# Optimization experiments

Hardware: AMD Instinct MI355X
Metric: run time of the kernel (lower is better)

Reference implementation:

```python
import jax, jax.numpy as jnp
import numpy as np

MAX_STEP = 20

def setup_inputs() -> dict:
    key = jax.random.key(0)
    k1, k2 = jax.random.split(key)
    B, L, E, H = 32, 2048, 256, 256
    word_rep = jax.random.normal(k1, (B, L, E), dtype=jnp.float32)
    # nn.Parameter(torch.randn(...).uniform_(-0.1, 0.1)) -> uniform in [-0.1, 0.1]
    cnn = jax.random.uniform(k2, (MAX_STEP, E, H), dtype=jnp.float32, minval=-0.1, maxval=0.1)
    return {"word_rep": word_rep, "cnn": cnn}

def reference(word_rep, cnn):
    # word_rep: [B, L, E]; cnn: [MAX_STEP, E, H]
    L = word_rep.shape[1]
    # Gather the cyclically-indexed per-position weight: [L, E, H]
    W = cnn[jnp.arange(L) % MAX_STEP]
    # Fused batched matmul over all positions at once: [B, L, H]
    hidden_vecs = jnp.einsum('ble,leh->blh', word_rep, W)
    return (hidden_vecs, hidden_vecs[:, -1])
```

## Files before the change

kernel.cpp:

```cpp
#include <hip/hip_runtime.h>
#include <hip/hip_bf16.h>

#define B_ 32
#define L_ 2048
#define E_ 256
#define H_ 256
#define MAXSTEP 20
#define NL 4
#define NCHUNK 26

typedef __attribute__((ext_vector_type(4))) float f32x4;
typedef __attribute__((ext_vector_type(8))) short bf16x8;
using bf16 = __hip_bfloat16;

__device__ inline short cvt1(float x) {
    bf16 b = __float2bfloat16(x);
    return *reinterpret_cast<short*>(&b);
}

__global__ void transpose_w_kernel(const float* __restrict__ cnn, short* __restrict__ wt) {
    __shared__ short tile[32][33];
    const int s  = blockIdx.z;
    const int e0 = blockIdx.y * 32;
    const int h0 = blockIdx.x * 32;
    const int tx = threadIdx.x;
    const int ty = threadIdx.y;
    const float* src = cnn + ((size_t)s * E_ + e0) * H_ + h0;
#pragma unroll
    for (int i = ty; i < 32; i += 8)
        tile[i][tx] = cvt1(src[(size_t)i * H_ + tx]);
    __syncthreads();
    short* dst = wt + ((size_t)s * H_ + h0) * E_ + e0;
#pragma unroll
    for (int i = ty; i < 32; i += 8)
        dst[(size_t)i * E_ + tx] = tile[tx][i];
}

__global__ __launch_bounds__(256, 2) void vaw_sames_kernel(
        const float* __restrict__ A, const short* __restrict__ Wt,
        float* __restrict__ out) {
    __shared__ __align__(16) float aLds[2][B_ * E_];

    const int s     = blockIdx.x / NCHUNK;
    const int chunk = blockIdx.x % NCHUNK;
    const int cnt   = (s < 8) ? 103 : 102;
    const int wv    = threadIdx.x >> 6;
    const int lane  = threadIdx.x & 63;
    const int r     = lane & 15;
    const int g     = lane >> 4;
    const int nbase = wv * 64;
    const int key   = r & 7;

    const short* wtb = Wt + ((size_t)s * H_ + nbase + r) * E_ + g * 8;
    bf16x8 breg[8][4];
#pragma unroll
    for (int kk = 0; kk < 8; ++kk)
#pragma unroll
        for (int nf = 0; nf < 4; ++nf)
            breg[kk][nf] = *(const bf16x8*)(wtb + (size_t)nf * 16 * E_ + kk * 32);

    auto lof = [&](int it) {
        int idx = chunk * NL + it;
        if (idx > cnt - 1) idx = cnt - 1;
        return s + 20 * idx;
    };

    auto stage = [&](int it) {
        const int l = lof(it);
        float* dst = aLds[it & 1];
#pragma unroll
        for (int t = 0; t < 8; ++t) {
            const int b  = t * 4 + wv;
            const int cg = lane ^ (b & 7);
            const float* gp = A + ((size_t)b * L_ + l) * E_ + cg * 4;
            __builtin_amdgcn_global_load_lds(
                (const __attribute__((address_space(1))) void*)gp,
                (__attribute__((address_space(3))) void*)&dst[b * 256],
                16, 0, 0);
        }
    };

    stage(0);

#pragma unroll
    for (int it = 0; it < NL; ++it) {
        const int l   = lof(it);
        const int cur = it & 1;

        if (it < NL - 1) stage(it + 1);
        if (it == 0)           asm volatile("s_waitcnt vmcnt(8)"  ::: "memory");
        else if (it < NL - 1)  asm volatile("s_waitcnt vmcnt(40)" ::: "memory");
        else                   asm volatile("s_waitcnt vmcnt(32)" ::: "memory");
        __builtin_amdgcn_s_barrier();
        __builtin_amdgcn_sched_barrier(0);

        f32x4 acc[2][4] = {};
#pragma unroll
        for (int kk = 0; kk < 8; ++kk) {
            const int c0 = kk * 8 + g * 2;
            f32x4 a0lo = *(const f32x4*)&aLds[cur][r * 256 + ((c0 ^ key) << 2)];
            f32x4 a0hi = *(const f32x4*)&aLds[cur][r * 256 + (((c0 + 1) ^ key) << 2)];
            f32x4 a1lo = *(const f32x4*)&aLds[cur][(r + 16) * 256 + ((c0 ^ key) << 2)];
            f32x4 a1hi = *(const f32x4*)&aLds[cur][(r + 16) * 256 + (((c0 + 1) ^ key) << 2)];
            bf16x8 a0, a1;
#pragma unroll
            for (int j = 0; j < 4; ++j) {
                a0[j]     = cvt1(a0lo[j]);
                a0[j + 4] = cvt1(a0hi[j]);
                a1[j]     = cvt1(a1lo[j]);
                a1[j + 4] = cvt1(a1hi[j]);
            }
#pragma unroll
            for (int nf = 0; nf < 4; ++nf) {
                acc[0][nf] = __builtin_amdgcn_mfma_f32_16x16x32_bf16(a0, breg[kk][nf], acc[0][nf], 0, 0, 0);
                acc[1][nf] = __builtin_amdgcn_mfma_f32_16x16x32_bf16(a1, breg[kk][nf], acc[1][nf], 0, 0, 0);
            }
        }

        const int row0 = g * 4;
#pragma unroll
        for (int mf = 0; mf < 2; ++mf) {
#pragma unroll
            for (int nf = 0; nf < 4; ++nf) {
                const int h = nbase + nf * 16 + r;
#pragma unroll
                for (int i = 0; i < 4; ++i) {
                    const int bb = mf * 16 + row0 + i;
                    out[((size_t)bb * L_ + l) * H_ + h] = acc[mf][nf][i];
                }
            }
        }
        if (l == L_ - 1) {
            float* out2 = out + (size_t)B_ * L_ * H_;
#pragma unroll
            for (int mf = 0; mf < 2; ++mf)
#pragma unroll
                for (int nf = 0; nf < 4; ++nf) {
                    const int h = nbase + nf * 16 + r;
#pragma unroll
                    for (int i = 0; i < 4; ++i) {
                        const int bb = mf * 16 + row0 + i;
                        out2[(size_t)bb * H_ + h] = acc[mf][nf][i];
                    }
                }
        }

        __builtin_amdgcn_s_barrier();
    }
}

__global__ __launch_bounds__(256) void vaw_fallback_kernel(
        const float* __restrict__ A, const float* __restrict__ W, float* __restrict__ out) {
    __shared__ __align__(16) float aLds[2][B_ * E_];
    const int l0   = blockIdx.x * NL;
    const int wv   = threadIdx.x >> 6;
    const int lane = threadIdx.x & 63;
    const int r    = lane & 15;
    const int g    = lane >> 4;
    const int nbase = wv * 64;
    const int key   = r & 7;

    auto stage = [&](int it) {
        float* dst = aLds[it & 1];
        const int l = l0 + it;
#pragma unroll
        for (int t = 0; t < 8; ++t) {
            const int b  = t * 4 + wv;
            const int cg = lane ^ (b & 7);
            const float* gp = A + ((size_t)b * L_ + l) * E_ + cg * 4;
            __builtin_amdgcn_global_load_lds(
                (const __attribute__((address_space(1))) void*)gp,
                (__attribute__((address_space(3))) void*)&dst[b * 256],
                16, 0, 0);
        }
    };

    stage(0);
#pragma unroll 1
    for (int it = 0; it < NL; ++it) {
        const int l   = l0 + it;
        const int sidx = l % MAXSTEP;
        const int cur = it & 1;
        if (it < NL - 1) {
            stage(it + 1);
            asm volatile("s_waitcnt vmcnt(8)" ::: "memory");
        } else {
            asm volatile("s_waitcnt vmcnt(0)" ::: "memory");
        }
        __builtin_amdgcn_s_barrier();
        __builtin_amdgcn_sched_barrier(0);

        f32x4 acc[2][4] = {};
        const float* Wf = W + (size_t)sidx * E_ * H_;
#pragma unroll 2
        for (int kk = 0; kk < 8; ++kk) {
            const int k0 = kk * 32;
            const int c0 = kk * 8 + g * 2;
            f32x4 a0lo = *(const f32x4*)&aLds[cur][r * 256 + ((c0 ^ key) << 2)];
            f32x4 a0hi = *(const f32x4*)&aLds[cur][r * 256 + (((c0 + 1) ^ key) << 2)];
            f32x4 a1lo = *(const f32x4*)&aLds[cur][(r + 16) * 256 + ((c0 ^ key) << 2)];
            f32x4 a1hi = *(const f32x4*)&aLds[cur][(r + 16) * 256 + (((c0 + 1) ^ key) << 2)];
            bf16x8 a0, a1;
#pragma unroll
            for (int j = 0; j < 4; ++j) {
                a0[j]     = cvt1(a0lo[j]);
                a0[j + 4] = cvt1(a0hi[j]);
                a1[j]     = cvt1(a1lo[j]);
                a1[j + 4] = cvt1(a1hi[j]);
            }
            bf16x8 b0, b1, b2, b3;
#pragma unroll
            for (int j = 0; j < 8; ++j) {
                const size_t krow = (size_t)(k0 + g * 8 + j) * H_;
                b0[j] = cvt1(Wf[krow + nbase +  0 + r]);
                b1[j] = cvt1(Wf[krow + nbase + 16 + r]);
                b2[j] = cvt1(Wf[krow + nbase + 32 + r]);
                b3[j] = cvt1(Wf[krow + nbase + 48 + r]);
            }
            acc[0][0] = __builtin_amdgcn_mfma_f32_16x16x32_bf16(a0, b0, acc[0][0], 0, 0, 0);
            acc[0][1] = __builtin_amdgcn_mfma_f32_16x16x32_bf16(a0, b1, acc[0][1], 0, 0, 0);
            acc[0][2] = __builtin_amdgcn_mfma_f32_16x16x32_bf16(a0, b2, acc[0][2], 0, 0, 0);
            acc[0][3] = __builtin_amdgcn_mfma_f32_16x16x32_bf16(a0, b3, acc[0][3], 0, 0, 0);
            acc[1][0] = __builtin_amdgcn_mfma_f32_16x16x32_bf16(a1, b0, acc[1][0], 0, 0, 0);
            acc[1][1] = __builtin_amdgcn_mfma_f32_16x16x32_bf16(a1, b1, acc[1][1], 0, 0, 0);
            acc[1][2] = __builtin_amdgcn_mfma_f32_16x16x32_bf16(a1, b2, acc[1][2], 0, 0, 0);
            acc[1][3] = __builtin_amdgcn_mfma_f32_16x16x32_bf16(a1, b3, acc[1][3], 0, 0, 0);
        }

        const int row0 = g * 4;
#pragma unroll
        for (int mf = 0; mf < 2; ++mf)
#pragma unroll
            for (int nf = 0; nf < 4; ++nf) {
                const int h = nbase + nf * 16 + r;
#pragma unroll
                for (int i = 0; i < 4; ++i) {
                    const int bb = mf * 16 + row0 + i;
                    out[((size_t)bb * L_ + l) * H_ + h] = acc[mf][nf][i];
                }
            }
        if (l == L_ - 1) {
            float* out2 = out + (size_t)B_ * L_ * H_;
#pragma unroll
            for (int mf = 0; mf < 2; ++mf)
#pragma unroll
                for (int nf = 0; nf < 4; ++nf) {
                    const int h = nbase + nf * 16 + r;
#pragma unroll
                    for (int i = 0; i < 4; ++i) {
                        const int bb = mf * 16 + row0 + i;
                        out2[(size_t)bb * H_ + h] = acc[mf][nf][i];
                    }
                }
        }
        __builtin_amdgcn_s_barrier();
    }
}

extern "C" void kernel_launch(void* const* d_in, const int* in_sizes, int n_in,
                              void* d_out, int out_size, void* d_ws, size_t ws_size,
                              hipStream_t stream) {
    const float* word_rep = (const float*)d_in[0];
    const float* cnn      = (const float*)d_in[1];
    float* out = (float*)d_out;

    const size_t wt_bytes = (size_t)MAXSTEP * E_ * H_ * sizeof(short);
    if (ws_size >= wt_bytes) {
        short* wt = (short*)d_ws;
        transpose_w_kernel<<<dim3(8, 8, 20), dim3(32, 8), 0, stream>>>(cnn, wt);
        vaw_sames_kernel<<<dim3(MAXSTEP * NCHUNK), dim3(256), 0, stream>>>(word_rep, wt, out);
    } else {
        vaw_fallback_kernel<<<dim3(L_ / NL), dim3(256), 0, stream>>>(word_rep, cnn, out);
    }
}
```

Baseline: 45.03 us.

## Split A staging into K-halves with triple-buffered LDS pipeline

Each position's activation tile is now staged in two halves along E (128 columns each) and rotated through three LDS buffers, with loads issued two stages ahead. Accumulators persist across the two halves, and results are stored only after the second half. LDS use per block drops from 64KB to 48KB, and load latency gets more overlap with MFMA work. The cost is twice as many barrier and wait steps per position, plus hand-tuned vmcnt values that must match exactly.

```diff
diff --git a/kernel.cpp b/kernel.cpp
--- a/kernel.cpp
+++ b/kernel.cpp
@@ -39,7 +39,7 @@
 __global__ __launch_bounds__(256, 2) void vaw_sames_kernel(
         const float* __restrict__ A, const short* __restrict__ Wt,
         float* __restrict__ out) {
-    __shared__ __align__(16) float aLds[2][B_ * E_];
+    __shared__ __align__(16) float aLds[3][B_ * 128];
 
     const int s     = blockIdx.x / NCHUNK;
     const int chunk = blockIdx.x % NCHUNK;
@@ -59,49 +59,67 @@
         for (int nf = 0; nf < 4; ++nf)
             breg[kk][nf] = *(const bf16x8*)(wtb + (size_t)nf * 16 * E_ + kk * 32);
 
-    auto lof = [&](int it) {
-        int idx = chunk * NL + it;
+    auto lof = [&](int il) {
+        int idx = chunk * NL + il;
         if (idx > cnt - 1) idx = cnt - 1;
         return s + 20 * idx;
     };
 
-    auto stage = [&](int it) {
-        const int l = lof(it);
-        float* dst = aLds[it & 1];
-#pragma unroll
-        for (int t = 0; t < 8; ++t) {
-            const int b  = t * 4 + wv;
-            const int cg = lane ^ (b & 7);
-            const float* gp = A + ((size_t)b * L_ + l) * E_ + cg * 4;
+    auto stage = [&](int t) {
+        const int l  = lof(t >> 1);
+        const int hk = t & 1;
+        float* dst = aLds[t % 3];
+        const int local = lane & 31;
+        const int half  = lane >> 5;
+#pragma unroll
+        for (int j = 0; j < 4; ++j) {
+            const int r0  = j * 8 + wv * 2;
+            const int row = r0 + half;
+            const int cg  = local ^ (row & 7);
+            const float* gp = A + ((size_t)row * L_ + l) * E_ + hk * 128 + cg * 4;
             __builtin_amdgcn_global_load_lds(
                 (const __attribute__((address_space(1))) void*)gp,
-                (__attribute__((address_space(3))) void*)&dst[b * 256],
+                (__attribute__((address_space(3))) void*)&dst[r0 * 128],
                 16, 0, 0);
         }
     };
 
     stage(0);
-
-#pragma unroll
-    for (int it = 0; it < NL; ++it) {
-        const int l   = lof(it);
-        const int cur = it & 1;
-
-        if (it < NL - 1) stage(it + 1);
-        if (it == 0)           asm volatile("s_waitcnt vmcnt(8)"  ::: "memory");
-        else if (it < NL - 1)  asm volatile("s_waitcnt vmcnt(40)" ::: "memory");
-        else                   asm volatile("s_waitcnt vmcnt(32)" ::: "memory");
+    stage(1);
+
+    f32x4 acc[2][4];
+
+#pragma unroll
+    for (int t = 0; t < 2 * NL; ++t) {
+        const int cur = t % 3;
+        const int hk  = t & 1;
+        const int l   = lof(t >> 1);
+
+        if (t < 2 * NL - 2) stage(t + 2);
+
+        if (t < 2)                asm volatile("s_waitcnt vmcnt(8)"  ::: "memory");
+        else if (t < 2 * NL - 2)  asm volatile("s_waitcnt vmcnt(40)" ::: "memory");
+        else if (t == 2 * NL - 2) asm volatile("s_waitcnt vmcnt(36)" ::: "memory");
+        else                      asm volatile("s_waitcnt vmcnt(32)" ::: "memory");
         __builtin_amdgcn_s_barrier();
         __builtin_amdgcn_sched_barrier(0);
 
-        f32x4 acc[2][4] = {};
-#pragma unroll
-        for (int kk = 0; kk < 8; ++kk) {
-            const int c0 = kk * 8 + g * 2;
-            f32x4 a0lo = *(const f32x4*)&aLds[cur][r * 256 + ((c0 ^ key) << 2)];
-            f32x4 a0hi = *(const f32x4*)&aLds[cur][r * 256 + (((c0 + 1) ^ key) << 2)];
-            f32x4 a1lo = *(const f32x4*)&aLds[cur][(r + 16) * 256 + ((c0 ^ key) << 2)];
-            f32x4 a1hi = *(const f32x4*)&aLds[cur][(r + 16) * 256 + (((c0 + 1) ^ key) << 2)];
+        if (hk == 0) {
+#pragma unroll
+            for (int mf = 0; mf < 2; ++mf)
+#pragma unroll
+                for (int nf = 0; nf < 4; ++nf)
+                    acc[mf][nf] = f32x4{0.f, 0.f, 0.f, 0.f};
+        }
+
+#pragma unroll
+        for (int kkh = 0; kkh < 4; ++kkh) {
+            const int kk = hk * 4 + kkh;
+            const int c0 = kkh * 8 + g * 2;
+            f32x4 a0lo = *(const f32x4*)&aLds[cur][r * 128 + ((c0 ^ key) << 2)];
+            f32x4 a0hi = *(const f32x4*)&aLds[cur][r * 128 + (((c0 + 1) ^ key) << 2)];
+            f32x4 a1lo = *(const f32x4*)&aLds[cur][(r + 16) * 128 + ((c0 ^ key) << 2)];
+            f32x4 a1hi = *(const f32x4*)&aLds[cur][(r + 16) * 128 + (((c0 + 1) ^ key) << 2)];
             bf16x8 a0, a1;
 #pragma unroll
             for (int j = 0; j < 4; ++j) {
@@ -117,32 +135,34 @@
             }
         }
 
-        const int row0 = g * 4;
-#pragma unroll
-        for (int mf = 0; mf < 2; ++mf) {
-#pragma unroll
-            for (int nf = 0; nf < 4; ++nf) {
-                const int h = nbase + nf * 16 + r;
-#pragma unroll
-                for (int i = 0; i < 4; ++i) {
-                    const int bb = mf * 16 + row0 + i;
-                    out[((size_t)bb * L_ + l) * H_ + h] = acc[mf][nf][i];
-                }
-            }
-        }
-        if (l == L_ - 1) {
-            float* out2 = out + (size_t)B_ * L_ * H_;
-#pragma unroll
-            for (int mf = 0; mf < 2; ++mf)
+        if (hk == 1) {
+            const int row0 = g * 4;
+#pragma unroll
+            for (int mf = 0; mf < 2; ++mf) {
 #pragma unroll
                 for (int nf = 0; nf < 4; ++nf) {
                     const int h = nbase + nf * 16 + r;
 #pragma unroll
                     for (int i = 0; i < 4; ++i) {
                         const int bb = mf * 16 + row0 + i;
-                        out2[(size_t)bb * H_ + h] = acc[mf][nf][i];
+                        out[((size_t)bb * L_ + l) * H_ + h] = acc[mf][nf][i];
                     }
                 }
+            }
+            if (l == L_ - 1) {
+                float* out2 = out + (size_t)B_ * L_ * H_;
+#pragma unroll
+                for (int mf = 0; mf < 2; ++mf)
+#pragma unroll
+                    for (int nf = 0; nf < 4; ++nf) {
+                        const int h = nbase + nf * 16 + r;
+#pragma unroll
+                        for (int i = 0; i < 4; ++i) {
+                            const int bb = mf * 16 + row0 + i;
+                            out2[(size_t)bb * H_ + h] = acc[mf][nf][i];
+                        }
+                    }
+            }
         }
 
         __builtin_amdgcn_s_barrier();
```

Measured after the change: 48.75 us. 1.08x slower.

## Split GEMM into single-wave blocks with triple-buffered K-slice pipeline

Applied to the files above, without the earlier changes.

Replaces the 4-wave block with independent 64-thread blocks, each computing a 64-column slice of H, and streams A in 64-wide K slices through a three-deep LDS ring without block barriers. This is meant to raise occupancy, shrink LDS use and remove barrier stalls. Each wave now loads the full A rows itself, so global A reads are quadrupled. The last-position output is moved to a separate small copy kernel.

```diff
diff --git a/kernel.cpp b/kernel.cpp
--- a/kernel.cpp
+++ b/kernel.cpp
@@ -6,8 +6,8 @@
 #define E_ 256
 #define H_ 256
 #define MAXSTEP 20
-#define NL 4
-#define NCHUNK 26
+#define NLW 4
+#define NCH 26
 
 typedef __attribute__((ext_vector_type(4))) float f32x4;
 typedef __attribute__((ext_vector_type(8))) short bf16x8;
@@ -36,19 +36,28 @@
         dst[(size_t)i * E_ + tx] = tile[tx][i];
 }
 
-__global__ __launch_bounds__(256, 2) void vaw_sames_kernel(
+__global__ void copy_last_kernel(const float* __restrict__ out, float* __restrict__ out2) {
+    const int h = threadIdx.x;
+#pragma unroll
+    for (int b = 0; b < B_; ++b)
+        out2[(size_t)b * H_ + h] = out[((size_t)b * L_ + (L_ - 1)) * H_ + h];
+}
+
+__global__ __launch_bounds__(64, 2) void vaw_wave_kernel(
         const float* __restrict__ A, const short* __restrict__ Wt,
         float* __restrict__ out) {
-    __shared__ __align__(16) float aLds[2][B_ * E_];
-
-    const int s     = blockIdx.x / NCHUNK;
-    const int chunk = blockIdx.x % NCHUNK;
+    __shared__ __align__(16) float aLds[3][B_ * 64];
+
+    const int bid   = blockIdx.x;
+    const int cg    = bid & 3;
+    const int sc    = bid >> 2;
+    const int s     = sc / NCH;
+    const int chunk = sc % NCH;
     const int cnt   = (s < 8) ? 103 : 102;
-    const int wv    = threadIdx.x >> 6;
-    const int lane  = threadIdx.x & 63;
+    const int lane  = threadIdx.x;
     const int r     = lane & 15;
     const int g     = lane >> 4;
-    const int nbase = wv * 64;
+    const int nbase = cg * 64;
     const int key   = r & 7;
 
     const short* wtb = Wt + ((size_t)s * H_ + nbase + r) * E_ + g * 8;
@@ -59,100 +68,117 @@
         for (int nf = 0; nf < 4; ++nf)
             breg[kk][nf] = *(const bf16x8*)(wtb + (size_t)nf * 16 * E_ + kk * 32);
 
-    auto lof = [&](int it) {
-        int idx = chunk * NL + it;
+    auto lof = [&](int il) {
+        int idx = chunk * NLW + il;
         if (idx > cnt - 1) idx = cnt - 1;
         return s + 20 * idx;
     };
 
-    auto stage = [&](int it) {
-        const int l = lof(it);
-        float* dst = aLds[it & 1];
-#pragma unroll
-        for (int t = 0; t < 8; ++t) {
-            const int b  = t * 4 + wv;
-            const int cg = lane ^ (b & 7);
-            const float* gp = A + ((size_t)b * L_ + l) * E_ + cg * 4;
+    auto stage = [&](int td) {
+        const int l  = lof(td >> 2);
+        const int kq = td & 3;
+        float* dst = aLds[td % 3];
+        const int row = (lane >> 4);
+        const int cL  = lane & 15;
+#pragma unroll
+        for (int j = 0; j < 8; ++j) {
+            const int rr = j * 4 + row;
+            const int cG = cL ^ (rr & 7);
+            const float* gp = A + ((size_t)rr * L_ + l) * E_ + kq * 64 + cG * 4;
             __builtin_amdgcn_global_load_lds(
                 (const __attribute__((address_space(1))) void*)gp,
-                (__attribute__((address_space(3))) void*)&dst[b * 256],
+                (__attribute__((address_space(3))) void*)&dst[j * 4 * 64],
                 16, 0, 0);
         }
     };
 
     stage(0);
-
-#pragma unroll
-    for (int it = 0; it < NL; ++it) {
-        const int l   = lof(it);
-        const int cur = it & 1;
-
-        if (it < NL - 1) stage(it + 1);
-        if (it == 0)           asm volatile("s_waitcnt vmcnt(8)"  ::: "memory");
-        else if (it < NL - 1)  asm volatile("s_waitcnt vmcnt(40)" ::: "memory");
-        else                   asm volatile("s_waitcnt vmcnt(32)" ::: "memory");
-        __builtin_amdgcn_s_barrier();
-        __builtin_amdgcn_sched_barrier(0);
-
-        f32x4 acc[2][4] = {};
-#pragma unroll
-        for (int kk = 0; kk < 8; ++kk) {
-            const int c0 = kk * 8 + g * 2;
-            f32x4 a0lo = *(const f32x4*)&aLds[cur][r * 256 + ((c0 ^ key) << 2)];
-            f32x4 a0hi = *(const f32x4*)&aLds[cur][r * 256 + (((c0 + 1) ^ key) << 2)];
-            f32x4 a1lo = *(const f32x4*)&aLds[cur][(r + 16) * 256 + ((c0 ^ key) << 2)];
-            f32x4 a1hi = *(const f32x4*)&aLds[cur][(r + 16) * 256 + (((c0 + 1) ^ key) << 2)];
-            bf16x8 a0, a1;
-#pragma unroll
-            for (int j = 0; j < 4; ++j) {
-                a0[j]     = cvt1(a0lo[j]);
-                a0[j + 4] = cvt1(a0hi[j]);
-                a1[j]     = cvt1(a1lo[j]);
-                a1[j + 4] = cvt1(a1hi[j]);
-            }
-#pragma unroll
-            for (int nf = 0; nf < 4; ++nf) {
-                acc[0][nf] = __builtin_amdgcn_mfma_f32_16x16x32_bf16(a0, breg[kk][nf], acc[0][nf], 0, 0, 0);
-                acc[1][nf] = __builtin_amdgcn_mfma_f32_16x16x32_bf16(a1, breg[kk][nf], acc[1][nf], 0, 0, 0);
-            }
-        }
-
-        const int row0 = g * 4;
-#pragma unroll
-        for (int mf = 0; mf < 2; ++mf) {
-#pragma unroll
-            for (int nf = 0; nf < 4; ++nf) {
-                const int h = nbase + nf * 16 + r;
-#pragma unroll
-                for (int i = 0; i < 4; ++i) {
-                    const int bb = mf * 16 + row0 + i;
-                    out[((size_t)bb * L_ + l) * H_ + h] = acc[mf][nf][i];
-                }
-            }
-        }
-        if (l == L_ - 1) {
-            float* out2 = out + (size_t)B_ * L_ * H_;
-#pragma unroll
-            for (int mf = 0; mf < 2; ++mf)
+    stage(1);
+
+    f32x4 acc[2][4];
+
+#pragma unroll 1
+    for (int il = 0; il < NLW; ++il) {
+        const int l     = lof(il);
+        const bool first = (il == 0);
+        const bool last  = (il == NLW - 1);
+
+#pragma unroll
+        for (int q = 0; q < 4; ++q) {
+            const int t   = il * 4 + q;
+            const int buf = t % 3;
+
+            if (!last || q < 2) stage(t + 2);
+
+            if (q == 0) {
+                if (first) asm volatile("s_waitcnt vmcnt(16)" ::: "memory");
+                else       asm volatile("s_waitcnt vmcnt(48)" ::: "memory");
+            } else if (q == 1) {
+                if (first) asm volatile("s_waitcnt vmcnt(16)" ::: "memory");
+                else       asm volatile("s_waitcnt vmcnt(48)" ::: "memory");
+            } else if (q == 2) {
+                if (last)  asm volatile("s_waitcnt vmcnt(8)"  ::: "memory");
+                else       asm volatile("s_waitcnt vmcnt(16)" ::: "memory");
+            } else {
+                if (last)  asm volatile("s_waitcnt vmcnt(0)"  ::: "memory");
+                else       asm volatile("s_waitcnt vmcnt(16)" ::: "memory");
+            }
+            __builtin_amdgcn_sched_barrier(0);
+
+            if (q == 0) {
+#pragma unroll
+                for (int mf = 0; mf < 2; ++mf)
+#pragma unroll
+                    for (int nf = 0; nf < 4; ++nf)
+                        acc[mf][nf] = f32x4{0.f, 0.f, 0.f, 0.f};
+            }
+
+#pragma unroll
+            for (int kkh = 0; kkh < 2; ++kkh) {
+                const int kk = q * 2 + kkh;
+                const int c0 = kkh * 8 + g * 2;
+                f32x4 a0lo = *(const f32x4*)&aLds[buf][r * 64 + ((c0 ^ key) << 2)];
+                f32x4 a0hi = *(const f32x4*)&aLds[buf][r * 64 + (((c0 + 1) ^ key) << 2)];
+                f32x4 a1lo = *(const f32x4*)&aLds[buf][(r + 16) * 64 + ((c0 ^ key) << 2)];
+                f32x4 a1hi = *(const f32x4*)&aLds[buf][(r + 16) * 64 + (((c0 + 1) ^ key) << 2)];
+                bf16x8 a0, a1;
+#pragma unroll
+                for (int j = 0; j < 4; ++j) {
+                    a0[j]     = cvt1(a0lo[j]);
+                    a0[j + 4] = cvt1(a0hi[j]);
+                    a1[j]     = cvt1(a1lo[j]);
+                    a1[j + 4] = cvt1(a1hi[j]);
+                }
 #pragma unroll
                 for (int nf = 0; nf < 4; ++nf) {
-                    const int h = nbase + nf * 16 + r;
-#pragma unroll
-                    for (int i = 0; i < 4; ++i) {
-                        const int bb = mf * 16 + row0 + i;
-                        out2[(size_t)bb * H_ + h] = acc[mf][nf][i];
+                    acc[0][nf] = __builtin_amdgcn_mfma_f32_16x16x32_bf16(a0, breg[kk][nf], acc[0][nf], 0, 0, 0);
+                    acc[1][nf] = __builtin_amdgcn_mfma_f32_16x16x32_bf16(a1, breg[kk][nf], acc[1][nf], 0, 0, 0);
+                }
+            }
+
+            if (q == 3) {
+                const int row0 = g * 4;
+#pragma unroll
+                for (int mf = 0; mf < 2; ++mf) {
+#pragma unroll
+                    for (int nf = 0; nf < 4; ++nf) {
+                        const int h = nbase + nf * 16 + r;
+#pragma unroll
+                        for (int i = 0; i < 4; ++i) {
+                            const int bb = mf * 16 + row0 + i;
+                            out[((size_t)bb * L_ + l) * H_ + h] = acc[mf][nf][i];
+                        }
                     }
                 }
-        }
-
-        __builtin_amdgcn_s_barrier();
+            }
+        }
     }
 }
 
 __global__ __launch_bounds__(256) void vaw_fallback_kernel(
         const float* __restrict__ A, const float* __restrict__ W, float* __restrict__ out) {
     __shared__ __align__(16) float aLds[2][B_ * E_];
-    const int l0   = blockIdx.x * NL;
+    const int l0   = blockIdx.x * 4;
     const int wv   = threadIdx.x >> 6;
     const int lane = threadIdx.x & 63;
     const int r    = lane & 15;
@@ -166,8 +192,8 @@
 #pragma unroll
         for (int t = 0; t < 8; ++t) {
             const int b  = t * 4 + wv;
-            const int cg = lane ^ (b & 7);
-            const float* gp = A + ((size_t)b * L_ + l) * E_ + cg * 4;
+            const int cgx = lane ^ (b & 7);
+            const float* gp = A + ((size_t)b * L_ + l) * E_ + cgx * 4;
             __builtin_amdgcn_global_load_lds(
                 (const __attribute__((address_space(1))) void*)gp,
                 (__attribute__((address_space(3))) void*)&dst[b * 256],
@@ -177,11 +203,11 @@
 
     stage(0);
 #pragma unroll 1
-    for (int it = 0; it < NL; ++it) {
+    for (int it = 0; it < 4; ++it) {
         const int l   = l0 + it;
         const int sidx = l % MAXSTEP;
         const int cur = it & 1;
-        if (it < NL - 1) {
+        if (it < 3) {
             stage(it + 1);
             asm volatile("s_waitcnt vmcnt(8)" ::: "memory");
         } else {
@@ -268,8 +294,9 @@
     if (ws_size >= wt_bytes) {
         short* wt = (short*)d_ws;
         transpose_w_kernel<<<dim3(8, 8, 20), dim3(32, 8), 0, stream>>>(cnn, wt);
-        vaw_sames_kernel<<<dim3(MAXSTEP * NCHUNK), dim3(256), 0, stream>>>(word_rep, wt, out);
+        vaw_wave_kernel<<<dim3(MAXSTEP * NCH * 4), dim3(64), 0, stream>>>(word_rep, wt, out);
+        copy_last_kernel<<<dim3(1), dim3(256), 0, stream>>>(out, out + (size_t)B_ * L_ * H_);
     } else {
-        vaw_fallback_kernel<<<dim3(L_ / NL), dim3(256), 0, stream>>>(word_rep, cnn, out);
+        vaw_fallback_kernel<<<dim3(L_ / 4), dim3(256), 0, stream>>>(word_rep, cnn, out);
     }
 }
```

Measured after the change: 64.63 us. +43.5%, slower.

## Split columns across eight waves per block to cut weight registers per wave

Applied to the files above, without the earlier changes.

The main kernel now runs 512 threads (8 waves) per block, with each wave owning 32 output columns instead of 64. This halves the per-wave weight register footprint and accumulators so more waves can be resident. The activation tile is loaded with 4 rows per wave, two stages are prefetched before the weight registers are filled, and the wait counts are retuned to match. The trade-off is that each wave converts the same A fragments for half as many MFMAs, so LDS reads and fp32-to-bf16 conversion per FLOP double.

```diff
diff --git a/kernel.cpp b/kernel.cpp
--- a/kernel.cpp
+++ b/kernel.cpp
@@ -7,7 +7,8 @@
 #define H_ 256
 #define MAXSTEP 20
 #define NL 4
-#define NCHUNK 26
+#define NCH 26
+#define NGRP (MAXSTEP * NCH)
 
 typedef __attribute__((ext_vector_type(4))) float f32x4;
 typedef __attribute__((ext_vector_type(8))) short bf16x8;
@@ -36,31 +37,24 @@
         dst[(size_t)i * E_ + tx] = tile[tx][i];
 }
 
-__global__ __launch_bounds__(256, 2) void vaw_sames_kernel(
+__global__ __launch_bounds__(512, 4) void vaw_occ_kernel(
         const float* __restrict__ A, const short* __restrict__ Wt,
         float* __restrict__ out) {
     __shared__ __align__(16) float aLds[2][B_ * E_];
 
-    const int s     = blockIdx.x / NCHUNK;
-    const int chunk = blockIdx.x % NCHUNK;
+    const int g_    = blockIdx.x;
+    const int s     = g_ / NCH;
+    const int chunk = g_ % NCH;
     const int cnt   = (s < 8) ? 103 : 102;
     const int wv    = threadIdx.x >> 6;
     const int lane  = threadIdx.x & 63;
     const int r     = lane & 15;
     const int g     = lane >> 4;
-    const int nbase = wv * 64;
+    const int nbase = wv * 32;
     const int key   = r & 7;
 
-    const short* wtb = Wt + ((size_t)s * H_ + nbase + r) * E_ + g * 8;
-    bf16x8 breg[8][4];
-#pragma unroll
-    for (int kk = 0; kk < 8; ++kk)
-#pragma unroll
-        for (int nf = 0; nf < 4; ++nf)
-            breg[kk][nf] = *(const bf16x8*)(wtb + (size_t)nf * 16 * E_ + kk * 32);
-
-    auto lof = [&](int it) {
-        int idx = chunk * NL + it;
+    auto lof = [&](int il) {
+        int idx = chunk * NL + il;
         if (idx > cnt - 1) idx = cnt - 1;
         return s + 20 * idx;
     };
@@ -69,32 +63,47 @@
         const int l = lof(it);
         float* dst = aLds[it & 1];
 #pragma unroll
-        for (int t = 0; t < 8; ++t) {
-            const int b  = t * 4 + wv;
-            const int cg = lane ^ (b & 7);
-            const float* gp = A + ((size_t)b * L_ + l) * E_ + cg * 4;
+        for (int j = 0; j < 4; ++j) {
+            const int row = wv + j * 8;
+            const int cg  = lane ^ (row & 7);
+            const float* gp = A + ((size_t)row * L_ + l) * E_ + cg * 4;
             __builtin_amdgcn_global_load_lds(
                 (const __attribute__((address_space(1))) void*)gp,
-                (__attribute__((address_space(3))) void*)&dst[b * 256],
+                (__attribute__((address_space(3))) void*)&dst[row * 256],
                 16, 0, 0);
         }
     };
 
     stage(0);
-
-#pragma unroll
+    stage(1);
+
+    const short* wtb = Wt + ((size_t)s * H_ + nbase + r) * E_ + g * 8;
+    bf16x8 breg[8][2];
+#pragma unroll
+    for (int kk = 0; kk < 8; ++kk)
+#pragma unroll
+        for (int nf = 0; nf < 2; ++nf)
+            breg[kk][nf] = *(const bf16x8*)(wtb + (size_t)nf * 16 * E_ + kk * 32);
+
+#pragma unroll 1
     for (int it = 0; it < NL; ++it) {
         const int l   = lof(it);
         const int cur = it & 1;
 
-        if (it < NL - 1) stage(it + 1);
-        if (it == 0)           asm volatile("s_waitcnt vmcnt(8)"  ::: "memory");
-        else if (it < NL - 1)  asm volatile("s_waitcnt vmcnt(40)" ::: "memory");
-        else                   asm volatile("s_waitcnt vmcnt(32)" ::: "memory");
+        if (it < NL - 1 && it >= 1) stage(it + 1);
+
+        if (it < NL - 1) asm volatile("s_waitcnt vmcnt(20)" ::: "memory");
+        else             asm volatile("s_waitcnt vmcnt(16)" ::: "memory");
         __builtin_amdgcn_s_barrier();
         __builtin_amdgcn_sched_barrier(0);
 
-        f32x4 acc[2][4] = {};
+        f32x4 acc[2][2];
+#pragma unroll
+        for (int mf = 0; mf < 2; ++mf)
+#pragma unroll
+            for (int nf = 0; nf < 2; ++nf)
+                acc[mf][nf] = f32x4{0.f, 0.f, 0.f, 0.f};
+
 #pragma unroll
         for (int kk = 0; kk < 8; ++kk) {
             const int c0 = kk * 8 + g * 2;
@@ -111,7 +120,7 @@
                 a1[j + 4] = cvt1(a1hi[j]);
             }
 #pragma unroll
-            for (int nf = 0; nf < 4; ++nf) {
+            for (int nf = 0; nf < 2; ++nf) {
                 acc[0][nf] = __builtin_amdgcn_mfma_f32_16x16x32_bf16(a0, breg[kk][nf], acc[0][nf], 0, 0, 0);
                 acc[1][nf] = __builtin_amdgcn_mfma_f32_16x16x32_bf16(a1, breg[kk][nf], acc[1][nf], 0, 0, 0);
             }
@@ -121,7 +130,7 @@
 #pragma unroll
         for (int mf = 0; mf < 2; ++mf) {
 #pragma unroll
-            for (int nf = 0; nf < 4; ++nf) {
+            for (int nf = 0; nf < 2; ++nf) {
                 const int h = nbase + nf * 16 + r;
 #pragma unroll
                 for (int i = 0; i < 4; ++i) {
@@ -135,7 +144,7 @@
 #pragma unroll
             for (int mf = 0; mf < 2; ++mf)
 #pragma unroll
-                for (int nf = 0; nf < 4; ++nf) {
+                for (int nf = 0; nf < 2; ++nf) {
                     const int h = nbase + nf * 16 + r;
 #pragma unroll
                     for (int i = 0; i < 4; ++i) {
@@ -152,7 +161,7 @@
 __global__ __launch_bounds__(256) void vaw_fallback_kernel(
         const float* __restrict__ A, const float* __restrict__ W, float* __restrict__ out) {
     __shared__ __align__(16) float aLds[2][B_ * E_];
-    const int l0   = blockIdx.x * NL;
+    const int l0   = blockIdx.x * 4;
     const int wv   = threadIdx.x >> 6;
     const int lane = threadIdx.x & 63;
     const int r    = lane & 15;
@@ -166,8 +175,8 @@
 #pragma unroll
         for (int t = 0; t < 8; ++t) {
             const int b  = t * 4 + wv;
-            const int cg = lane ^ (b & 7);
-            const float* gp = A + ((size_t)b * L_ + l) * E_ + cg * 4;
+            const int cgx = lane ^ (b & 7);
+            const float* gp = A + ((size_t)b * L_ + l) * E_ + cgx * 4;
             __builtin_amdgcn_global_load_lds(
                 (const __attribute__((address_space(1))) void*)gp,
                 (__attribute__((address_space(3))) void*)&dst[b * 256],
@@ -177,11 +186,11 @@
 
     stage(0);
 #pragma unroll 1
-    for (int it = 0; it < NL; ++it) {
+    for (int it = 0; it < 4; ++it) {
         const int l   = l0 + it;
         const int sidx = l % MAXSTEP;
         const int cur = it & 1;
-        if (it < NL - 1) {
+        if (it < 3) {
             stage(it + 1);
             asm volatile("s_waitcnt vmcnt(8)" ::: "memory");
         } else {
@@ -268,8 +277,8 @@
     if (ws_size >= wt_bytes) {
         short* wt = (short*)d_ws;
         transpose_w_kernel<<<dim3(8, 8, 20), dim3(32, 8), 0, stream>>>(cnn, wt);
-        vaw_sames_kernel<<<dim3(MAXSTEP * NCHUNK), dim3(256), 0, stream>>>(word_rep, wt, out);
+        vaw_occ_kernel<<<dim3(NGRP), dim3(512), 0, stream>>>(word_rep, wt, out);
     } else {
-        vaw_fallback_kernel<<<dim3(L_ / NL), dim3(256), 0, stream>>>(word_rep, cnn, out);
+        vaw_fallback_kernel<<<dim3(L_ / 4), dim3(256), 0, stream>>>(word_rep, cnn, out);
     }
 }
```

Result: slower. 55.85 us (+24.0%).
